# Performance work log

Hardware: AMD Instinct MI355X
Metric: run time of the kernel (lower is better)

## Reference

```python
import jax, jax.numpy as jnp
import numpy as np

B, C, U = 8, 32, 32
K = 5            # powers = k + 1 with k = 4
N1, N2 = 256, 256


def setup_inputs() -> dict:
    key = jax.random.key(0)
    k_x, k_c1, k_c2, k_w = jax.random.split(key, 4)
    x = jax.random.normal(k_x, (B, C, N1, N2), dtype=jnp.float32)
    # Chebyshev polynomial bases T_0..T_k of the (rescaled) Laplacians of the
    # two factor graphs; registered buffers in the torch module.
    cheb1 = jax.random.normal(k_c1, (K, N1, N1), dtype=jnp.float32)
    cheb2 = jax.random.normal(k_c2, (K, N2, N2), dtype=jnp.float32)
    # Trainable anisotropic coefficients [powers, powers, channels, units],
    # initialized N(0, 0.001) in the original module.
    coefs = jax.random.normal(k_w, (K, K, C, U), dtype=jnp.float32) * 0.001
    return {"x": x, "cheb1": cheb1, "cheb2": cheb2, "coefs": coefs}


def reference(x, cheb1, cheb2, coefs):
    """Fused form of the anisotropic Chebyshev convolution.

    Original triple loop computes
      out[b,u,m,n] = sum_{k1,k2,i,p,q}
          coefs[k1,k2,i,u] * cheb1[k1,p,m] * cheb2[k2,q,n] * x[b,i,p,q]
    """
    # Filter along the first graph axis for every power k1: [B, K, C, N1, N2]
    a = jnp.einsum('kpm,bipq->bkimq', cheb1, x)
    # Contract channels and k1 with the learned coefficients: [B, K, U, N1, N2]
    c = jnp.einsum('bkimq,kliu->blumq', a, coefs)
    # Filter along the second graph axis for every power k2: [B, U, N1, N2]
    out = jnp.einsum('blumq,lqn->bumn', c, cheb2)
    return out
```

## Files before the change

### kernel.cpp

```cpp
#include <hip/hip_runtime.h>
#include <stdint.h>

#define WB 8
#define WC 32
#define WU 32
#define WK 5
#define WN 256
#define NN 65536
#define KC 160
#define KQ 1280

typedef __attribute__((ext_vector_type(8))) short bf8;
typedef __attribute__((ext_vector_type(8))) unsigned short us8;
typedef __attribute__((ext_vector_type(4))) float f4;

__device__ __forceinline__ unsigned short f2b(float f) {
    union { float f; uint32_t u; } v; v.f = f;
    uint32_t u = v.u;
    return (unsigned short)((u + 0x7FFFu + ((u >> 16) & 1u)) >> 16);
}

__device__ __forceinline__ void gload16(const unsigned short* g, unsigned short* l) {
    __builtin_amdgcn_global_load_lds(
        (const __attribute__((address_space(1))) unsigned int*)g,
        (__attribute__((address_space(3))) unsigned int*)l, 16, 0, 0);
}

__global__ void prep_small(const float* __restrict__ cheb1,
                           const float* __restrict__ cheb2,
                           const float* __restrict__ coefs,
                           unsigned short* __restrict__ c1T,
                           unsigned short* __restrict__ c2T,
                           unsigned short* __restrict__ Wt) {
    int idx = blockIdx.x * 256 + threadIdx.x;
    if (idx < WK * NN) {
        int k = idx / NN, r = idx % NN, m = r / WN, p = r % WN;
        c1T[idx] = f2b(cheb1[(k * WN + p) * WN + m]);
    }
    if (idx < WN * KQ) {
        int n = idx / KQ, r = idx % KQ;
        c2T[idx] = f2b(cheb2[r * WN + n]);
    }
    if (idx < KC * KC) {
        int lu = idx / KC, ki = idx % KC;
        int l = lu >> 5, u = lu & 31, k = ki >> 5, i = ki & 31;
        Wt[idx] = f2b(coefs[((k * WK + l) * WC + i) * WU + u]);
    }
}

__global__ void prep_x(const float* __restrict__ x, unsigned short* __restrict__ xT) {
    __shared__ unsigned short tile[64][72];
    int bi = blockIdx.z;
    int p0 = blockIdx.y * 64, q0 = blockIdx.x * 64;
    const float* src = x + (size_t)bi * NN;
    unsigned short* dst = xT + (size_t)bi * NN;
    int t = threadIdx.x;
    int c4 = (t & 15) * 4, r0 = t >> 4;
    for (int it = 0; it < 4; ++it) {
        int r = r0 + it * 16;
        float4 v = *reinterpret_cast<const float4*>(&src[(size_t)(p0 + r) * WN + q0 + c4]);
        tile[r][c4 + 0] = f2b(v.x); tile[r][c4 + 1] = f2b(v.y);
        tile[r][c4 + 2] = f2b(v.z); tile[r][c4 + 3] = f2b(v.w);
    }
    __syncthreads();
    for (int it = 0; it < 4; ++it) {
        int q = r0 + it * 16;
        ushort4 o;
        o.x = tile[c4 + 0][q]; o.y = tile[c4 + 1][q];
        o.z = tile[c4 + 2][q]; o.w = tile[c4 + 3][q];
        *reinterpret_cast<ushort4*>(&dst[(size_t)(q0 + q) * WN + p0 + c4]) = o;
    }
}

__global__ __launch_bounds__(512, 4) void g1(const unsigned short* __restrict__ c1T,
                                             const unsigned short* __restrict__ xT,
                                             unsigned short* __restrict__ a, int b_base) {
    __shared__ unsigned short As[128 * 64];
    __shared__ unsigned short Bs[256 * 64];
    int z = blockIdx.y;
    int bl = z >> 5, i = z & 31;
    int row0 = blockIdx.x * 128;
    int b = b_base + bl;
    const unsigned short* Asrc = c1T;
    const unsigned short* Bsrc = xT + (size_t)(b * WC + i) * NN;
    unsigned short* Out = a + (size_t)bl * KC * NN;

    int t = threadIdx.x;
    int w = t >> 6, l = t & 63;
    int wm = (w >> 2) * 64, wn = (w & 3) * 64;
    int lr = l & 15, hi = l >> 4;
    int srow = l >> 3;
    int scol = ((l & 7) ^ srow) * 8;

    f4 acc[4][4];
    for (int mf = 0; mf < 4; ++mf) for (int nf = 0; nf < 4; ++nf) acc[mf][nf] = (f4)(0.0f);

    for (int p0 = 0; p0 < 256; p0 += 64) {
        __syncthreads();
        for (int it = 0; it < 2; ++it) {
            int chunk = it * 8 + w;
            int row = chunk * 8 + srow;
            gload16(&Asrc[(size_t)(row0 + row) * 256 + p0 + scol], &As[chunk * 512]);
        }
        for (int it = 0; it < 4; ++it) {
            int chunk = it * 8 + w;
            int row = chunk * 8 + srow;
            gload16(&Bsrc[(size_t)row * 256 + p0 + scol], &Bs[chunk * 512]);
        }
        __syncthreads();
        for (int kk = 0; kk < 2; ++kk) {
            bf8 af[4], bfr[4];
            for (int mf = 0; mf < 4; ++mf) {
                int r = wm + mf * 16 + lr;
                af[mf] = *(const bf8*)&As[r * 64 + (((kk * 4 + hi) ^ (r & 7)) * 8)];
            }
            for (int nf = 0; nf < 4; ++nf) {
                int rb = wn + nf * 16 + lr;
                bfr[nf] = *(const bf8*)&Bs[rb * 64 + (((kk * 4 + hi) ^ (rb & 7)) * 8)];
            }
            for (int mf = 0; mf < 4; ++mf)
                for (int nf = 0; nf < 4; ++nf)
                    acc[mf][nf] = __builtin_amdgcn_mfma_f32_16x16x32_bf16(af[mf], bfr[nf], acc[mf][nf], 0, 0, 0);
        }
    }
    for (int mf = 0; mf < 4; ++mf)
        for (int nf = 0; nf < 4; ++nf)
            for (int j = 0; j < 4; ++j) {
                int grow = row0 + wm + mf * 16 + hi * 4 + j;
                int k = grow >> 8, m = grow & 255;
                int q = wn + nf * 16 + lr;
                Out[(size_t)(k * 32 + i) * NN + m * 256 + q] = f2b(acc[mf][nf][j]);
            }
}

__global__ __launch_bounds__(512, 4) void g2p(const unsigned short* __restrict__ Wt,
                                              const unsigned short* __restrict__ a,
                                              unsigned short* __restrict__ c) {
    __shared__ unsigned short Bt[128 * 172];
    int bl = blockIdx.y;
    int n0 = blockIdx.x * 128;
    const unsigned short* asrc = a + (size_t)bl * KC * NN;
    unsigned short* Out = c + (size_t)bl * KC * NN;
    int t = threadIdx.x;

    for (int s = 0; s < 2; ++s) {
        int task = t + s * 512;
        if (task < 640) {
            int oct = task & 15, kq = task >> 4;
            const unsigned short* src = asrc + (size_t)(kq * 4) * NN + n0 + oct * 8;
            us8 v0 = *(const us8*)&src[0 * NN];
            us8 v1 = *(const us8*)&src[1 * NN];
            us8 v2 = *(const us8*)&src[2 * NN];
            us8 v3 = *(const us8*)&src[3 * NN];
            #pragma unroll
            for (int j = 0; j < 8; ++j) {
                ushort4 wv;
                wv.x = v0[j]; wv.y = v1[j]; wv.z = v2[j]; wv.w = v3[j];
                *reinterpret_cast<ushort4*>(&Bt[(oct * 8 + j) * 172 + kq * 4]) = wv;
            }
        }
    }
    __syncthreads();

    int w = t >> 6, l = t & 63;
    int mh = w >> 2, nq = w & 3;
    int lr = l & 15, hi = l >> 4;
    f4 acc[5][2];
    for (int mf = 0; mf < 5; ++mf) { acc[mf][0] = (f4)(0.0f); acc[mf][1] = (f4)(0.0f); }

    for (int kk = 0; kk < 5; ++kk) {
        int k0 = kk * 32 + hi * 8;
        bf8 bfr[2];
        #pragma unroll
        for (int nf = 0; nf < 2; ++nf) {
            int pix = (nq * 2 + nf) * 16 + lr;
            typedef __attribute__((ext_vector_type(4))) short s4v;
            s4v lo  = *(const s4v*)&Bt[pix * 172 + k0];
            s4v hi4 = *(const s4v*)&Bt[pix * 172 + k0 + 4];
            bfr[nf] = __builtin_shufflevector(lo, hi4, 0, 1, 2, 3, 4, 5, 6, 7);
        }
        #pragma unroll
        for (int mf = 0; mf < 5; ++mf) {
            int row = mh * 80 + mf * 16 + lr;
            bf8 afr = *(const bf8*)&Wt[(size_t)row * KC + k0];
            acc[mf][0] = __builtin_amdgcn_mfma_f32_16x16x32_bf16(afr, bfr[0], acc[mf][0], 0, 0, 0);
            acc[mf][1] = __builtin_amdgcn_mfma_f32_16x16x32_bf16(afr, bfr[1], acc[mf][1], 0, 0, 0);
        }
    }
    for (int mf = 0; mf < 5; ++mf)
        for (int nf = 0; nf < 2; ++nf)
            for (int j = 0; j < 4; ++j) {
                int row = mh * 80 + mf * 16 + hi * 4 + j;
                int col = n0 + (nq * 2 + nf) * 16 + lr;
                Out[(size_t)row * NN + col] = f2b(acc[mf][nf][j]);
            }
}

__global__ __launch_bounds__(512, 4) void g3(const unsigned short* __restrict__ c,
                                             const unsigned short* __restrict__ c2T,
                                             float* __restrict__ out, int b_base) {
    __shared__ unsigned short As[2][128 * 64];
    __shared__ unsigned short Bs[256 * 64];
    int bl = blockIdx.y;
    int b = b_base + bl;
    int R0 = blockIdx.x * 128;
    int u = R0 >> 8, m0 = R0 & 255;
    const unsigned short* Csrc = c + (size_t)bl * KC * NN;

    int t = threadIdx.x;
    int w = t >> 6, l = t & 63;
    int wm = (w >> 2) * 64, wn = (w & 3) * 64;
    int lr = l & 15, hi = l >> 4;
    int srow = l >> 3;
    int scol = ((l & 7) ^ srow) * 8;

    f4 acc[4][4];
    for (int mf = 0; mf < 4; ++mf) for (int nf = 0; nf < 4; ++nf) acc[mf][nf] = (f4)(0.0f);

#define G3_STAGE_A(buf, step) do { \
    int lq_ = (step) >> 2, q0_ = ((step) & 3) * 64; \
    const unsigned short* Arow0 = Csrc + (size_t)(lq_ * 32 + u) * NN + (size_t)m0 * 256 + q0_; \
    for (int it = 0; it < 2; ++it) { \
        int chunk = it * 8 + w; int row = chunk * 8 + srow; \
        gload16(&Arow0[(size_t)row * 256 + scol], &As[buf][chunk * 512]); } \
} while (0)
#define G3_STAGE_B(step) do { \
    const unsigned short* Brow0 = c2T + (step) * 64; \
    for (int it = 0; it < 4; ++it) { \
        int chunk = it * 8 + w; int row = chunk * 8 + srow; \
        gload16(&Brow0[(size_t)row * KQ + scol], &Bs[chunk * 512]); } \
} while (0)

    G3_STAGE_A(0, 0);
    for (int step = 0; step < 20; ++step) {
        int cur = step & 1;
        G3_STAGE_B(step);
        if (step < 19) {
            G3_STAGE_A(cur ^ 1, step + 1);
            asm volatile("s_waitcnt vmcnt(2)" ::: "memory");
        } else {
            asm volatile("s_waitcnt vmcnt(0)" ::: "memory");
        }
        __builtin_amdgcn_s_barrier();
        asm volatile("" ::: "memory");
        for (int kk = 0; kk < 2; ++kk) {
            bf8 af[4], bfr[4];
            for (int mf = 0; mf < 4; ++mf) {
                int r = wm + mf * 16 + lr;
                af[mf] = *(const bf8*)&As[cur][r * 64 + (((kk * 4 + hi) ^ (r & 7)) * 8)];
            }
            for (int nf = 0; nf < 4; ++nf) {
                int rb = wn + nf * 16 + lr;
                bfr[nf] = *(const bf8*)&Bs[rb * 64 + (((kk * 4 + hi) ^ (rb & 7)) * 8)];
            }
            for (int mf = 0; mf < 4; ++mf)
                for (int nf = 0; nf < 4; ++nf)
                    acc[mf][nf] = __builtin_amdgcn_mfma_f32_16x16x32_bf16(af[mf], bfr[nf], acc[mf][nf], 0, 0, 0);
        }
        asm volatile("" ::: "memory");
        __builtin_amdgcn_s_barrier();
    }
#undef G3_STAGE_A
#undef G3_STAGE_B
    for (int mf = 0; mf < 4; ++mf)
        for (int nf = 0; nf < 4; ++nf)
            for (int j = 0; j < 4; ++j) {
                int m = m0 + wm + mf * 16 + hi * 4 + j;
                int n = wn + nf * 16 + lr;
                out[((size_t)(b * WU + u) * WN + m) * WN + n] = acc[mf][nf][j];
            }
}

extern "C" void kernel_launch(void* const* d_in, const int* in_sizes, int n_in,
                              void* d_out, int out_size, void* d_ws, size_t ws_size,
                              hipStream_t stream) {
    const float* x     = (const float*)d_in[0];
    const float* cheb1 = (const float*)d_in[1];
    const float* cheb2 = (const float*)d_in[2];
    const float* coefs = (const float*)d_in[3];
    float* out = (float*)d_out;
    unsigned short* ws = (unsigned short*)d_ws;

    size_t off = 0;
    unsigned short* xT  = ws + off; off += (size_t)WB * WC * NN;
    unsigned short* c1T = ws + off; off += (size_t)WK * NN;
    unsigned short* c2T = ws + off; off += (size_t)WN * KQ;
    unsigned short* Wt  = ws + off; off += (size_t)KC * KC;
    size_t fixed_elems = off;
    size_t a1 = (size_t)KC * NN;

    prep_small<<<1280, 256, 0, stream>>>(cheb1, cheb2, coefs, c1T, c2T, Wt);
    prep_x<<<dim3(4, 4, WB * WC), 256, 0, stream>>>(x, xT);

    size_t avail = ws_size / 2;
    size_t rem = avail > fixed_elems ? avail - fixed_elems : 0;

    if (rem >= 9 * a1) {
        int nb = (int)((rem - 8 * a1) / a1);
        if (nb < 1) nb = 1;
        if (nb > WB) nb = WB;
        unsigned short* a_ = ws + fixed_elems;
        unsigned short* c_ = a_ + (size_t)nb * a1;
        for (int b0 = 0; b0 < WB; b0 += nb) {
            int cur = (WB - b0 < nb) ? (WB - b0) : nb;
            g1<<<dim3(10, cur * 32), 512, 0, stream>>>(c1T, xT, a_, b0);
            g2p<<<dim3(512, cur), 512, 0, stream>>>(Wt, a_, c_ + (size_t)b0 * a1);
        }
        g3<<<dim3(64, WB), 512, 0, stream>>>(c_, c2T, out, 0);
    } else {
        size_t per_b = 2 * a1;
        int nb = (int)(rem / per_b);
        if (nb < 1) nb = 1;
        if (nb > WB) nb = WB;
        unsigned short* a_ = ws + fixed_elems;
        unsigned short* c_ = a_ + (size_t)nb * a1;
        for (int b0 = 0; b0 < WB; b0 += nb) {
            int cur = (WB - b0 < nb) ? (WB - b0) : nb;
            g1<<<dim3(10, cur * 32), 512, 0, stream>>>(c1T, xT, a_, b0);
            g2p<<<dim3(512, cur), 512, 0, stream>>>(Wt, a_, c_);
            g3<<<dim3(64, cur), 512, 0, stream>>>(c_, c2T, out, b0);
        }
    }
}
```

Before: 286.6 us.

## Double-buffer A tile in g1 and remap blocks for XCD-local reuse

The g1 GEMM now double-buffers the Chebyshev A tile in LDS. The next A tile is prefetched while the current B tile loads, and explicit vmcnt waits plus barriers replace the plain syncthreads. The launch grid is flattened to 1D and block indices are remapped so that the ten row-blocks sharing one x slice land on the same XCD, which should improve L2 reuse of that slice. The extra LDS buffer raises shared-memory use per block, and the hand-written waitcnt logic depends on the load count per thread.

```diff
diff --git a/kernel.cpp b/kernel.cpp
--- a/kernel.cpp
+++ b/kernel.cpp
@@ -75,11 +75,15 @@
 __global__ __launch_bounds__(512, 4) void g1(const unsigned short* __restrict__ c1T,
                                              const unsigned short* __restrict__ xT,
                                              unsigned short* __restrict__ a, int b_base) {
-    __shared__ unsigned short As[128 * 64];
+    __shared__ unsigned short As[2][128 * 64];
     __shared__ unsigned short Bs[256 * 64];
-    int z = blockIdx.y;
-    int bl = z >> 5, i = z & 31;
-    int row0 = blockIdx.x * 128;
+    int p = blockIdx.x;
+    int gpx = gridDim.x / 80;
+    int xcd = p & 7, j = p >> 3;
+    int grp = xcd * gpx + j / 10;
+    int member = j % 10;
+    int bl = grp >> 5, i = grp & 31;
+    int row0 = member * 128;
     int b = b_base + bl;
     const unsigned short* Asrc = c1T;
     const unsigned short* Bsrc = xT + (size_t)(b * WC + i) * NN;
@@ -95,24 +99,36 @@
     f4 acc[4][4];
     for (int mf = 0; mf < 4; ++mf) for (int nf = 0; nf < 4; ++nf) acc[mf][nf] = (f4)(0.0f);
 
-    for (int p0 = 0; p0 < 256; p0 += 64) {
-        __syncthreads();
-        for (int it = 0; it < 2; ++it) {
-            int chunk = it * 8 + w;
-            int row = chunk * 8 + srow;
-            gload16(&Asrc[(size_t)(row0 + row) * 256 + p0 + scol], &As[chunk * 512]);
-        }
-        for (int it = 0; it < 4; ++it) {
-            int chunk = it * 8 + w;
-            int row = chunk * 8 + srow;
-            gload16(&Bsrc[(size_t)row * 256 + p0 + scol], &Bs[chunk * 512]);
-        }
-        __syncthreads();
+#define G1_STAGE_A(buf, step) do { \
+    int p0_ = (step) * 64; \
+    for (int it = 0; it < 2; ++it) { \
+        int chunk = it * 8 + w; int row = chunk * 8 + srow; \
+        gload16(&Asrc[(size_t)(row0 + row) * 256 + p0_ + scol], &As[buf][chunk * 512]); } \
+} while (0)
+#define G1_STAGE_B(step) do { \
+    int p0_ = (step) * 64; \
+    for (int it = 0; it < 4; ++it) { \
+        int chunk = it * 8 + w; int row = chunk * 8 + srow; \
+        gload16(&Bsrc[(size_t)row * 256 + p0_ + scol], &Bs[chunk * 512]); } \
+} while (0)
+
+    G1_STAGE_A(0, 0);
+    for (int step = 0; step < 4; ++step) {
+        int cur = step & 1;
+        G1_STAGE_B(step);
+        if (step < 3) {
+            G1_STAGE_A(cur ^ 1, step + 1);
+            asm volatile("s_waitcnt vmcnt(2)" ::: "memory");
+        } else {
+            asm volatile("s_waitcnt vmcnt(0)" ::: "memory");
+        }
+        __builtin_amdgcn_s_barrier();
+        asm volatile("" ::: "memory");
         for (int kk = 0; kk < 2; ++kk) {
             bf8 af[4], bfr[4];
             for (int mf = 0; mf < 4; ++mf) {
                 int r = wm + mf * 16 + lr;
-                af[mf] = *(const bf8*)&As[r * 64 + (((kk * 4 + hi) ^ (r & 7)) * 8)];
+                af[mf] = *(const bf8*)&As[cur][r * 64 + (((kk * 4 + hi) ^ (r & 7)) * 8)];
             }
             for (int nf = 0; nf < 4; ++nf) {
                 int rb = wn + nf * 16 + lr;
@@ -122,14 +138,18 @@
                 for (int nf = 0; nf < 4; ++nf)
                     acc[mf][nf] = __builtin_amdgcn_mfma_f32_16x16x32_bf16(af[mf], bfr[nf], acc[mf][nf], 0, 0, 0);
         }
-    }
+        asm volatile("" ::: "memory");
+        __builtin_amdgcn_s_barrier();
+    }
+#undef G1_STAGE_A
+#undef G1_STAGE_B
     for (int mf = 0; mf < 4; ++mf)
         for (int nf = 0; nf < 4; ++nf)
-            for (int j = 0; j < 4; ++j) {
-                int grow = row0 + wm + mf * 16 + hi * 4 + j;
+            for (int j2 = 0; j2 < 4; ++j2) {
+                int grow = row0 + wm + mf * 16 + hi * 4 + j2;
                 int k = grow >> 8, m = grow & 255;
                 int q = wn + nf * 16 + lr;
-                Out[(size_t)(k * 32 + i) * NN + m * 256 + q] = f2b(acc[mf][nf][j]);
+                Out[(size_t)(k * 32 + i) * NN + m * 256 + q] = f2b(acc[mf][nf][j2]);
             }
 }
 
@@ -303,7 +323,7 @@
         unsigned short* c_ = a_ + (size_t)nb * a1;
         for (int b0 = 0; b0 < WB; b0 += nb) {
             int cur = (WB - b0 < nb) ? (WB - b0) : nb;
-            g1<<<dim3(10, cur * 32), 512, 0, stream>>>(c1T, xT, a_, b0);
+            g1<<<dim3(cur * 320), 512, 0, stream>>>(c1T, xT, a_, b0);
             g2p<<<dim3(512, cur), 512, 0, stream>>>(Wt, a_, c_ + (size_t)b0 * a1);
         }
         g3<<<dim3(64, WB), 512, 0, stream>>>(c_, c2T, out, 0);
@@ -316,7 +336,7 @@
         unsigned short* c_ = a_ + (size_t)nb * a1;
         for (int b0 = 0; b0 < WB; b0 += nb) {
             int cur = (WB - b0 < nb) ? (WB - b0) : nb;
-            g1<<<dim3(10, cur * 32), 512, 0, stream>>>(c1T, xT, a_, b0);
+            g1<<<dim3(cur * 320), 512, 0, stream>>>(c1T, xT, a_, b0);
             g2p<<<dim3(512, cur), 512, 0, stream>>>(Wt, a_, c_);
             g3<<<dim3(64, cur), 512, 0, stream>>>(c_, c2T, out, b0);
         }
```

After: 280.4 us. 1.02x faster.
